# Optimization experiments

Hardware: AMD Instinct MI355X
Metric: run time of the kernel (lower is better)

## Reference

```python
import jax, jax.numpy as jnp
import numpy as np

B, D, L, NH = 8, 1024, 1024, 8
DK = D // NH  # = Dv = 128
NEG = -1e30


def setup_inputs() -> dict:
    key = jax.random.key(0)
    kx, km, kq, kk, kv, ko = jax.random.split(key, 6)
    x = jax.random.normal(kx, (B, D, L), dtype=jnp.float32)
    # binary mask over sequence positions (float, as in the torch code)
    mask = (jax.random.uniform(km, (B, L)) > 0.1).astype(jnp.float32)
    # xavier-ish scale for per-head projections, kaiming-ish for Wo
    s_qkv = np.sqrt(2.0 / (D + DK)).astype(np.float32)
    Wq = jax.random.normal(kq, (NH, D, DK), dtype=jnp.float32) * s_qkv
    Wk = jax.random.normal(kk, (NH, D, DK), dtype=jnp.float32) * s_qkv
    Wv = jax.random.normal(kv, (NH, D, DK), dtype=jnp.float32) * s_qkv
    Wo = jax.random.normal(ko, (D, DK * NH), dtype=jnp.float32) * np.sqrt(2.0 / D).astype(np.float32)
    return {"x": x, "mask": mask, "Wq": Wq, "Wk": Wk, "Wv": Wv, "Wo": Wo}


def reference(x, mask, Wq, Wk, Wv, Wo):
    # x: [B, D, L] -> [B, L, D]
    xt = jnp.swapaxes(x, 1, 2)
    scale = 1.0 / np.sqrt(DK).astype(np.float32)
    # batched per-head projections (equivalent to the per-head loop)
    q = jnp.einsum("bld,hdk->bhlk", xt, Wq)  # [B,H,L,Dk]
    k = jnp.einsum("bld,hdk->bhlk", xt, Wk)
    v = jnp.einsum("bld,hdk->bhlk", xt, Wv)
    # scores[b,h,q_pos,k_pos]
    scores = jnp.einsum("bhqd,bhkd->bhqk", q, k) * scale
    # mask.unsqueeze(2) in torch -> additive mask along the QUERY axis
    scores = scores + (1.0 - mask)[:, None, :, None] * NEG
    # faithful quirk: softmax over dim=1 of [B,Lq,Lk] == query axis (axis=2 here)
    attn = jax.nn.softmax(scores, axis=2)
    heads = jnp.einsum("bhqk,bhkd->bhqd", attn, v)  # [B,H,L,Dv]
    head = jnp.swapaxes(heads, 1, 2).reshape(B, L, NH * DK)  # concat heads
    out = head @ Wo  # [B, L, D]
    return jnp.swapaxes(out, 1, 2)  # [B, D, L]
```

## Files before the change

kernel.cpp:

```cpp
#include <hip/hip_runtime.h>

typedef short bf16x8 __attribute__((ext_vector_type(8)));
typedef float f32x4 __attribute__((ext_vector_type(4)));

#define MASK_NEG (-1e30f)

__device__ __forceinline__ unsigned short f2bf(float f) {
  union { float f; unsigned u; } v; v.f = f;
  unsigned r = v.u + 0x7fffu + ((v.u >> 16) & 1u);
  return (unsigned short)(r >> 16);
}

__device__ __forceinline__ float bf2f(unsigned short u) {
  union { unsigned u; float f; } v; v.u = ((unsigned)u) << 16;
  return v.f;
}

__device__ __forceinline__ void gl_lds16(const void* g, void* l) {
  __builtin_amdgcn_global_load_lds(
      (__attribute__((address_space(1))) void*)(void*)g,
      (__attribute__((address_space(3))) void*)l, 16, 0, 0);
}

__device__ __forceinline__ void transpose_tile(
    const float* __restrict__ s, unsigned short* __restrict__ d,
    int R, int C, int x0, int y0, int t, float tile[64][65]) {
  {
    const int r = t >> 4, c4 = (t & 15) * 4;
    for (int it = 0; it < 4; ++it) {
      const int rr = r + it * 16;
      const float4 v = *(const float4*)(s + (size_t)(y0 + rr) * C + x0 + c4);
      tile[rr][c4 + 0] = v.x; tile[rr][c4 + 1] = v.y;
      tile[rr][c4 + 2] = v.z; tile[rr][c4 + 3] = v.w;
    }
  }
  __syncthreads();
  {
    const int cc = t >> 4, r4 = (t & 15) * 4;
    for (int it = 0; it < 4; ++it) {
      const int c = cc + it * 16;
      ushort4 o;
      o.x = f2bf(tile[r4 + 0][c]); o.y = f2bf(tile[r4 + 1][c]);
      o.z = f2bf(tile[r4 + 2][c]); o.w = f2bf(tile[r4 + 3][c]);
      *(ushort4*)(d + (size_t)(x0 + c) * R + y0 + r4) = o;
    }
  }
}

__global__ __launch_bounds__(256) void transpose_x_wo(
    const float* __restrict__ x, const float* __restrict__ Wo,
    unsigned short* __restrict__ xt, unsigned short* __restrict__ Wot) {
  __shared__ float tile[64][65];
  const int z = blockIdx.z;
  const float* s = (z < 8) ? (x + (size_t)z * 1048576) : Wo;
  unsigned short* d = (z < 8) ? (xt + (size_t)z * 1048576) : Wot;
  transpose_tile(s, d, 1024, 1024, blockIdx.x * 64, blockIdx.y * 64,
                 threadIdx.x, tile);
}

__global__ __launch_bounds__(256) void transpose_w24(
    const float* __restrict__ Wq, const float* __restrict__ Wk,
    const float* __restrict__ Wv, unsigned short* __restrict__ WqkvT) {
  __shared__ float tile[64][65];
  const int z = blockIdx.z;
  const int sel = z >> 3, h = z & 7;
  const float* base = (sel == 0) ? Wq : (sel == 1) ? Wk : Wv;
  const float* s = base + (size_t)h * 131072;
  unsigned short* d = WqkvT + (size_t)z * 131072;
  transpose_tile(s, d, 1024, 128, blockIdx.x * 64, blockIdx.y * 64,
                 threadIdx.x, tile);
}

template<bool F32OUT>
__global__ __launch_bounds__(256) void gemm_tn(
    const unsigned short* __restrict__ A, const unsigned short* __restrict__ B,
    void* __restrict__ Cv,
    int K, int ldA, int ldB, int ldC, float scale,
    long sAl, long sAb, long sAh,
    long sBl, long sBb, long sBh,
    long sCl, long sCb, long sCh,
    int zbase, int zdiv)
{
  __shared__ unsigned short As[128 * 64];
  __shared__ unsigned short Bs[128 * 64];
  int bx, by, bz;
  {
    const int nx = gridDim.x, ny = gridDim.y;
    const int nwg = nx * ny * gridDim.z;
    int flat = blockIdx.x + nx * (blockIdx.y + ny * blockIdx.z);
    if ((nwg & 7) == 0) flat = (flat & 7) * (nwg >> 3) + (flat >> 3);
    bx = flat % nx; flat /= nx;
    by = flat % ny; bz = flat / ny;
  }
  const int z = bz;
  const int g = zbase + z;
  const int gb = g / zdiv, gh = g % zdiv;
  const unsigned short* Ab = A + (size_t)z * sAl + (size_t)gb * sAb + (size_t)gh * sAh;
  const unsigned short* Bb = B + (size_t)z * sBl + (size_t)gb * sBb + (size_t)gh * sBh;
  const int m0 = by * 128, n0 = bx * 128;
  const int t = threadIdx.x;
  const int lane = t & 63;
  const int wave = t >> 6;
  const int wm = wave >> 1, wn = wave & 1;

  const int sr2 = t >> 3;
  const int ss8 = t & 7;
  const int sq8 = ss8 ^ (sr2 & 7);

  const unsigned short* ap0 = Ab + (size_t)(m0 +  0 + sr2) * ldA + sq8 * 8;
  const unsigned short* ap1 = Ab + (size_t)(m0 + 32 + sr2) * ldA + sq8 * 8;
  const unsigned short* ap2 = Ab + (size_t)(m0 + 64 + sr2) * ldA + sq8 * 8;
  const unsigned short* ap3 = Ab + (size_t)(m0 + 96 + sr2) * ldA + sq8 * 8;
  const unsigned short* bp0 = Bb + (size_t)(n0 +  0 + sr2) * ldB + sq8 * 8;
  const unsigned short* bp1 = Bb + (size_t)(n0 + 32 + sr2) * ldB + sq8 * 8;
  const unsigned short* bp2 = Bb + (size_t)(n0 + 64 + sr2) * ldB + sq8 * 8;
  const unsigned short* bp3 = Bb + (size_t)(n0 + 96 + sr2) * ldB + sq8 * 8;

  char* asd0 = (char*)As +     0 + t * 16;
  char* asd1 = (char*)As +  4096 + t * 16;
  char* asd2 = (char*)As +  8192 + t * 16;
  char* asd3 = (char*)As + 12288 + t * 16;
  char* bsd0 = (char*)Bs +     0 + t * 16;
  char* bsd1 = (char*)Bs +  4096 + t * 16;
  char* bsd2 = (char*)Bs +  8192 + t * 16;
  char* bsd3 = (char*)Bs + 12288 + t * 16;

  const int tq = lane & 15, qd = lane >> 4;

  f32x4 acc[4][4];
  #pragma unroll
  for (int i = 0; i < 4; ++i)
    #pragma unroll
    for (int j = 0; j < 4; ++j)
      acc[i][j] = f32x4{0.f, 0.f, 0.f, 0.f};

  const int kIters = K >> 6;
  for (int kt = 0; kt < kIters; ++kt) {
    __syncthreads();
    gl_lds16(ap0, asd0); gl_lds16(ap1, asd1);
    gl_lds16(ap2, asd2); gl_lds16(ap3, asd3);
    gl_lds16(bp0, bsd0); gl_lds16(bp1, bsd1);
    gl_lds16(bp2, bsd2); gl_lds16(bp3, bsd3);
    ap0 += 64; ap1 += 64; ap2 += 64; ap3 += 64;
    bp0 += 64; bp1 += 64; bp2 += 64; bp3 += 64;
    __builtin_amdgcn_s_waitcnt(0x0f70);
    __syncthreads();

    #pragma unroll
    for (int kk = 0; kk < 2; ++kk) {
      bf16x8 af[4], bfr[4];
      #pragma unroll
      for (int i = 0; i < 4; ++i) {
        const int R = wm * 64 + i * 16 + tq;
        const int slot = (kk * 4 + qd) ^ (R & 7);
        af[i] = *(const bf16x8*)(As + R * 64 + slot * 8);
      }
      #pragma unroll
      for (int j = 0; j < 4; ++j) {
        const int R = wn * 64 + j * 16 + tq;
        const int slot = (kk * 4 + qd) ^ (R & 7);
        bfr[j] = *(const bf16x8*)(Bs + R * 64 + slot * 8);
      }
      #pragma unroll
      for (int i = 0; i < 4; ++i)
        #pragma unroll
        for (int j = 0; j < 4; ++j)
          acc[i][j] = __builtin_amdgcn_mfma_f32_16x16x32_bf16(af[i], bfr[j], acc[i][j], 0, 0, 0);
    }
  }

  const size_t cOff = (size_t)z * sCl + (size_t)gb * sCb + (size_t)gh * sCh;
  #pragma unroll
  for (int i = 0; i < 4; ++i) {
    const int row = m0 + wm * 64 + i * 16 + qd * 4;
    #pragma unroll
    for (int j = 0; j < 4; ++j) {
      const int col = n0 + wn * 64 + j * 16 + tq;
      if constexpr (F32OUT) {
        float* C = (float*)Cv + cOff;
        #pragma unroll
        for (int rr = 0; rr < 4; ++rr)
          C[(size_t)(row + rr) * ldC + col] = acc[i][j][rr] * scale;
      } else {
        unsigned short* C = (unsigned short*)Cv + cOff;
        #pragma unroll
        for (int rr = 0; rr < 4; ++rr)
          C[(size_t)(row + rr) * ldC + col] = f2bf(acc[i][j][rr] * scale);
      }
    }
  }
}

__global__ __launch_bounds__(256) void gemm_scores_colsum(
    const unsigned short* __restrict__ QKV, float* __restrict__ colsum,
    const float* __restrict__ mask)
{
  __shared__ unsigned short sbuf[32768];
  unsigned short* As = sbuf;
  unsigned short* Bs = sbuf + 16384;
  int flat = blockIdx.x + 8 * (blockIdx.y + 8 * blockIdx.z);
  flat = (flat & 7) * 512 + (flat >> 3);
  const int bx = flat & 7, by = (flat >> 3) & 7, g = flat >> 6;
  const int b = g >> 3, h = g & 7;
  const unsigned short* Ab = QKV + (size_t)b * 3145728 + (size_t)h * 131072;
  const unsigned short* Bb = Ab + 1048576;
  const int m0 = by * 128, n0 = bx * 128;
  const int t = threadIdx.x;
  const int lane = t & 63;
  const int wave = t >> 6;
  const int wm = wave >> 1, wn = wave & 1;
  const int tq = lane & 15, qd = lane >> 4;

  const unsigned short* Aq = Ab + (size_t)m0 * 128;
  const unsigned short* Bk = Bb + (size_t)n0 * 128;
  #pragma unroll
  for (int it = 0; it < 8; ++it) {
    const int c = it * 256 + t;
    const int row = c >> 4;
    const int src = (c ^ (c >> 4)) & 15;
    gl_lds16(Aq + (size_t)row * 128 + src * 8, (char*)As + c * 16);
    gl_lds16(Bk + (size_t)row * 128 + src * 8, (char*)Bs + c * 16);
  }
  __builtin_amdgcn_s_waitcnt(0x0f70);
  __syncthreads();

  f32x4 acc[4][4];
  #pragma unroll
  for (int i = 0; i < 4; ++i)
    #pragma unroll
    for (int j = 0; j < 4; ++j)
      acc[i][j] = f32x4{0.f, 0.f, 0.f, 0.f};

  #pragma unroll
  for (int kk = 0; kk < 4; ++kk) {
    bf16x8 af[4], bfr[4];
    #pragma unroll
    for (int i = 0; i < 4; ++i) {
      const int R = wm * 64 + i * 16 + tq;
      const int slot = (kk * 4 + qd) ^ (R & 15);
      af[i] = *(const bf16x8*)(As + R * 128 + slot * 8);
    }
    #pragma unroll
    for (int j = 0; j < 4; ++j) {
      const int R = wn * 64 + j * 16 + tq;
      const int slot = (kk * 4 + qd) ^ (R & 15);
      bfr[j] = *(const bf16x8*)(Bs + R * 128 + slot * 8);
    }
    #pragma unroll
    for (int i = 0; i < 4; ++i)
      #pragma unroll
      for (int j = 0; j < 4; ++j)
        acc[i][j] = __builtin_amdgcn_mfma_f32_16x16x32_bf16(af[i], bfr[j], acc[i][j], 0, 0, 0);
  }

  float* cs = colsum + (size_t)g * 1024;
  const float scl = 0.08838834764831845f;
  const float* mrow = mask + (size_t)b * 1024;

  float cp[4] = {0.f, 0.f, 0.f, 0.f};
  #pragma unroll
  for (int i = 0; i < 4; ++i) {
    const int r0 = wm * 64 + i * 16 + qd * 4;
    const float4 m4 = *(const float4*)(mrow + m0 + r0);
    const float aq[4] = {(1.f - m4.x) * MASK_NEG - 20.f, (1.f - m4.y) * MASK_NEG - 20.f,
                         (1.f - m4.z) * MASK_NEG - 20.f, (1.f - m4.w) * MASK_NEG - 20.f};
    #pragma unroll
    for (int rr = 0; rr < 4; ++rr) {
      #pragma unroll
      for (int j = 0; j < 4; ++j) {
        const float e = __expf(acc[i][j][rr] * scl + aq[rr]);
        cp[j] += e;
      }
    }
  }
  #pragma unroll
  for (int j = 0; j < 4; ++j) {
    float v = cp[j];
    v += __shfl_xor(v, 16, 64);
    v += __shfl_xor(v, 32, 64);
    if (qd == 0)
      atomicAdd(&cs[n0 + wn * 64 + j * 16 + tq], v);
  }
}

__global__ __launch_bounds__(256) void tvscale(
    const unsigned short* __restrict__ QKV, unsigned short* __restrict__ Vp,
    const float* __restrict__ colsum)
{
  __shared__ unsigned short tile[64][72];
  const int g = blockIdx.z;
  const int b = g >> 3, h = g & 7;
  const unsigned short* S = QKV + (size_t)b * 3145728 + (size_t)(16 + h) * 131072;
  unsigned short* D = Vp + (size_t)g * 131072;
  const float* cs = colsum + (size_t)g * 1024;
  const int l0 = blockIdx.x * 64;
  const int d0 = blockIdx.y * 64;
  const int t = threadIdx.x;
  {
    const int r = t >> 4, c4 = (t & 15) * 4;
    for (int it = 0; it < 4; ++it) {
      const int rr = r + it * 16;
      const ushort4 v = *(const ushort4*)(S + (size_t)(l0 + rr) * 128 + d0 + c4);
      *(ushort4*)&tile[rr][c4] = v;
    }
  }
  __syncthreads();
  {
    const int cc = t >> 4, r4 = (t & 15) * 4;
    const float4 c4v = *(const float4*)(cs + l0 + r4);
    for (int it = 0; it < 4; ++it) {
      const int c = cc + it * 16;
      ushort4 o;
      o.x = f2bf(bf2f(tile[r4 + 0][c]) / c4v.x);
      o.y = f2bf(bf2f(tile[r4 + 1][c]) / c4v.y);
      o.z = f2bf(bf2f(tile[r4 + 2][c]) / c4v.z);
      o.w = f2bf(bf2f(tile[r4 + 3][c]) / c4v.w);
      *(ushort4*)(D + (size_t)(d0 + c) * 1024 + l0 + r4) = o;
    }
  }
}

__global__ __launch_bounds__(256, 2) void attn_pv_fused(
    const unsigned short* __restrict__ QKV, const unsigned short* __restrict__ Vp,
    unsigned short* __restrict__ Hp, const float* __restrict__ mask)
{
  __shared__ unsigned short lds[32768];
  unsigned short* Qs = lds;
  unsigned short* Ps = lds;
  unsigned short* Ks = lds + 16384;
  unsigned short* Vs = lds + 24576;

  const int bid = blockIdx.x;
  const int w = ((bid & 7) << 6) | (bid >> 3);
  const int g = w >> 3, qx = w & 7;
  const int b = g >> 3, h = g & 7;
  const unsigned short* Qg = QKV + (size_t)b * 3145728 + (size_t)h * 131072
                                 + (size_t)qx * 16384;
  const unsigned short* Kg = QKV + (size_t)b * 3145728 + (size_t)(8 + h) * 131072;
  const unsigned short* Vg = Vp + (size_t)g * 131072;

  const int t = threadIdx.x;
  const int lane = t & 63, wave = t >> 6;
  const int wm = wave >> 1, wn = wave & 1;
  const int tq = lane & 15, qd = lane >> 4;

  #pragma unroll
  for (int it = 0; it < 8; ++it) {
    const int c = it * 256 + t;
    const int row = c >> 4;
    const int src = (c ^ (c >> 4)) & 15;
    gl_lds16(Qg + (size_t)row * 128 + src * 8, (char*)Qs + c * 16);
  }
  __builtin_amdgcn_s_waitcnt(0x0f70);
  __syncthreads();

  bf16x8 qf[4][4];
  #pragma unroll
  for (int i = 0; i < 4; ++i) {
    const int R = wm * 64 + i * 16 + tq;
    #pragma unroll
    for (int kk = 0; kk < 4; ++kk)
      qf[i][kk] = *(const bf16x8*)(Qs + R * 128 + (((kk * 4 + qd) ^ (R & 15)) * 8));
  }
  __syncthreads();

  f32x4 acc_h[4][4];
  #pragma unroll
  for (int i = 0; i < 4; ++i)
    #pragma unroll
    for (int j = 0; j < 4; ++j)
      acc_h[i][j] = f32x4{0.f, 0.f, 0.f, 0.f};

  const float scl = 0.08838834764831845f;
  float aq[4][4];
  {
    const float* mrow = mask + (size_t)b * 1024 + qx * 128;
    #pragma unroll
    for (int i = 0; i < 4; ++i) {
      const float4 m4 = *(const float4*)(mrow + wm * 64 + i * 16 + qd * 4);
      aq[i][0] = (1.f - m4.x) * MASK_NEG - 20.f;
      aq[i][1] = (1.f - m4.y) * MASK_NEG - 20.f;
      aq[i][2] = (1.f - m4.z) * MASK_NEG - 20.f;
      aq[i][3] = (1.f - m4.w) * MASK_NEG - 20.f;
    }
  }

  for (int kt = 0; kt < 16; ++kt) {
    __syncthreads();
    #pragma unroll
    for (int it = 0; it < 4; ++it) {
      const int c = it * 256 + t;
      const int row = c >> 4;
      const int src = (c ^ (c >> 4)) & 15;
      gl_lds16(Kg + (size_t)(kt * 64 + row) * 128 + src * 8, (char*)Ks + c * 16);
    }
    #pragma unroll
    for (int it = 0; it < 4; ++it) {
      const int c = it * 256 + t;
      const int row = c >> 3;
      const int src = (c ^ (c >> 3)) & 7;
      gl_lds16(Vg + (size_t)row * 1024 + kt * 64 + src * 8, (char*)Vs + c * 16);
    }
    __builtin_amdgcn_s_waitcnt(0x0f70);
    __syncthreads();

    f32x4 acc_s[4][2];
    #pragma unroll
    for (int i = 0; i < 4; ++i)
      #pragma unroll
      for (int j = 0; j < 2; ++j)
        acc_s[i][j] = f32x4{0.f, 0.f, 0.f, 0.f};
    #pragma unroll
    for (int kk = 0; kk < 4; ++kk) {
      bf16x8 kf[2];
      #pragma unroll
      for (int j = 0; j < 2; ++j) {
        const int R = wn * 32 + j * 16 + tq;
        kf[j] = *(const bf16x8*)(Ks + R * 128 + (((kk * 4 + qd) ^ (R & 15)) * 8));
      }
      #pragma unroll
      for (int i = 0; i < 4; ++i)
        #pragma unroll
        for (int j = 0; j < 2; ++j)
          acc_s[i][j] = __builtin_amdgcn_mfma_f32_16x16x32_bf16(qf[i][kk], kf[j], acc_s[i][j], 0, 0, 0);
    }

    #pragma unroll
    for (int i = 0; i < 4; ++i) {
      const int q0 = wm * 64 + i * 16 + qd * 4;
      #pragma unroll
      for (int rr = 0; rr < 4; ++rr) {
        const int q = q0 + rr;
        #pragma unroll
        for (int j = 0; j < 2; ++j) {
          const int kl = wn * 32 + j * 16 + tq;
          const float e = __expf(acc_s[i][j][rr] * scl + aq[i][rr]);
          Ps[q * 64 + ((((kl >> 3) ^ (q & 7)) * 8) | (kl & 7))] = f2bf(e);
        }
      }
    }
    __syncthreads();

    #pragma unroll
    for (int k2 = 0; k2 < 2; ++k2) {
      bf16x8 pf[4], vf[4];
      #pragma unroll
      for (int i = 0; i < 4; ++i) {
        const int R = wm * 64 + i * 16 + tq;
        pf[i] = *(const bf16x8*)(Ps + R * 64 + (((k2 * 4 + qd) ^ (R & 7)) * 8));
      }
      #pragma unroll
      for (int j = 0; j < 4; ++j) {
        const int R = wn * 64 + j * 16 + tq;
        vf[j] = *(const bf16x8*)(Vs + R * 64 + (((k2 * 4 + qd) ^ (R & 7)) * 8));
      }
      #pragma unroll
      for (int i = 0; i < 4; ++i)
        #pragma unroll
        for (int j = 0; j < 4; ++j)
          acc_h[i][j] = __builtin_amdgcn_mfma_f32_16x16x32_bf16(pf[i], vf[j], acc_h[i][j], 0, 0, 0);
    }
  }

  unsigned short* Hb = Hp + (size_t)b * 1048576 + (size_t)qx * 131072 + h * 128;
  #pragma unroll
  for (int i = 0; i < 4; ++i) {
    const int q0 = wm * 64 + i * 16 + qd * 4;
    #pragma unroll
    for (int j = 0; j < 4; ++j) {
      const int dv = wn * 64 + j * 16 + tq;
      #pragma unroll
      for (int rr = 0; rr < 4; ++rr)
        Hb[(size_t)(q0 + rr) * 1024 + dv] = f2bf(acc_h[i][j][rr]);
    }
  }
}

extern "C" void kernel_launch(void* const* d_in, const int* in_sizes, int n_in,
                              void* d_out, int out_size, void* d_ws, size_t ws_size,
                              hipStream_t stream) {
  const float* x    = (const float*)d_in[0];
  const float* mask = (const float*)d_in[1];
  const float* Wq   = (const float*)d_in[2];
  const float* Wk   = (const float*)d_in[3];
  const float* Wv   = (const float*)d_in[4];
  const float* Wo   = (const float*)d_in[5];
  float* out = (float*)d_out;

  char* p = (char*)d_ws;
  unsigned short* xt    = (unsigned short*)p; p += 16777216;
  unsigned short* WqkvT = (unsigned short*)p; p += 6291456;
  unsigned short* Wot   = (unsigned short*)p; p += 2097152;
  unsigned short* QKV   = (unsigned short*)p; p += 50331648;
  unsigned short* Vp    = (unsigned short*)p; p += 16777216;
  unsigned short* Hp    = (unsigned short*)p; p += 16777216;
  float* colsum = (float*)p; p += 262144;

  hipMemsetAsync(colsum, 0, 262144, stream);

  transpose_x_wo<<<dim3(16, 16, 9), 256, 0, stream>>>(x, Wo, xt, Wot);
  transpose_w24<<<dim3(2, 16, 24), 256, 0, stream>>>(Wq, Wk, Wv, WqkvT);

  gemm_tn<false><<<dim3(1, 8, 192), 256, 0, stream>>>(
      xt, WqkvT, (void*)QKV, 1024, 1024, 1024, 128, 1.f,
      0L, 1048576L, 0L,  0L, 0L, 131072L,  0L, 3145728L, 131072L, 0, 24);

  gemm_scores_colsum<<<dim3(8, 8, 64), 256, 0, stream>>>(QKV, colsum, mask);

  tvscale<<<dim3(16, 2, 64), 256, 0, stream>>>(QKV, Vp, colsum);

  attn_pv_fused<<<dim3(512, 1, 1), 256, 0, stream>>>(QKV, Vp, Hp, mask);

  gemm_tn<true><<<dim3(8, 8, 8), 256, 0, stream>>>(
      Wot, Hp, (void*)out, 1024, 1024, 1024, 1024, 1.f,
      0L, 0L, 0L,  0L, 1048576L, 0L,  0L, 1048576L, 0L, 0, 1);
}
```

Measured before the change: 276.2 us.

## Fuse V transpose into QKV GEMM and fold colsum scaling into attention

The QKV projection GEMM now writes V directly in transposed layout, so the separate tvscale kernel goes away. The per-key column-sum normalization moves into the attention kernel, which multiplies each exp by the reciprocal colsum. The scores/colsum kernel is restructured to loop over K tiles per query block with double-buffered loads, and the attention kernel double-buffers its K/V loads to overlap them with compute. The costs are more LDS per block, uncoalesced ushort4 transposed stores in the GEMM epilogue, and more atomics per block in the colsum pass.

```diff
diff --git a/kernel.cpp b/kernel.cpp
--- a/kernel.cpp
+++ b/kernel.cpp
@@ -9,11 +9,6 @@
   union { float f; unsigned u; } v; v.f = f;
   unsigned r = v.u + 0x7fffu + ((v.u >> 16) & 1u);
   return (unsigned short)(r >> 16);
-}
-
-__device__ __forceinline__ float bf2f(unsigned short u) {
-  union { unsigned u; float f; } v; v.u = ((unsigned)u) << 16;
-  return v.f;
 }
 
 __device__ __forceinline__ void gl_lds16(const void* g, void* l) {
@@ -79,7 +74,7 @@
     long sAl, long sAb, long sAh,
     long sBl, long sBb, long sBh,
     long sCl, long sCb, long sCh,
-    int zbase, int zdiv)
+    int zbase, int zdiv, unsigned short* __restrict__ Vt)
 {
   __shared__ unsigned short As[128 * 64];
   __shared__ unsigned short Bs[128 * 64];
@@ -169,6 +164,25 @@
     }
   }
 
+  if (!F32OUT && Vt != nullptr && gh >= 16) {
+    unsigned short* Vb = Vt + (size_t)(gb * 8 + (gh - 16)) * 131072;
+    #pragma unroll
+    for (int i = 0; i < 4; ++i) {
+      const int row = m0 + wm * 64 + i * 16 + qd * 4;
+      #pragma unroll
+      for (int j = 0; j < 4; ++j) {
+        const int col = n0 + wn * 64 + j * 16 + tq;
+        ushort4 o;
+        o.x = f2bf(acc[i][j][0] * scale);
+        o.y = f2bf(acc[i][j][1] * scale);
+        o.z = f2bf(acc[i][j][2] * scale);
+        o.w = f2bf(acc[i][j][3] * scale);
+        *(ushort4*)(Vb + (size_t)col * 1024 + row) = o;
+      }
+    }
+    return;
+  }
+
   const size_t cOff = (size_t)z * sCl + (size_t)gb * sCb + (size_t)gh * sCh;
   #pragma unroll
   for (int i = 0; i < 4; ++i) {
@@ -191,144 +205,133 @@
   }
 }
 
-__global__ __launch_bounds__(256) void gemm_scores_colsum(
+__global__ __launch_bounds__(256, 2) void scores_colsum(
     const unsigned short* __restrict__ QKV, float* __restrict__ colsum,
     const float* __restrict__ mask)
 {
-  __shared__ unsigned short sbuf[32768];
-  unsigned short* As = sbuf;
-  unsigned short* Bs = sbuf + 16384;
-  int flat = blockIdx.x + 8 * (blockIdx.y + 8 * blockIdx.z);
-  flat = (flat & 7) * 512 + (flat >> 3);
-  const int bx = flat & 7, by = (flat >> 3) & 7, g = flat >> 6;
+  __shared__ unsigned short lds[24576];
+  unsigned short* Qs = lds;
+
+  const int bid = blockIdx.x;
+  const int w = ((bid & 7) << 6) | (bid >> 3);
+  const int g = w >> 3, qx = w & 7;
   const int b = g >> 3, h = g & 7;
-  const unsigned short* Ab = QKV + (size_t)b * 3145728 + (size_t)h * 131072;
-  const unsigned short* Bb = Ab + 1048576;
-  const int m0 = by * 128, n0 = bx * 128;
+  const unsigned short* Qg = QKV + (size_t)b * 3145728 + (size_t)h * 131072
+                                 + (size_t)qx * 16384;
+  const unsigned short* Kg = QKV + (size_t)b * 3145728 + (size_t)(8 + h) * 131072;
+
   const int t = threadIdx.x;
-  const int lane = t & 63;
-  const int wave = t >> 6;
+  const int lane = t & 63, wave = t >> 6;
   const int wm = wave >> 1, wn = wave & 1;
   const int tq = lane & 15, qd = lane >> 4;
 
-  const unsigned short* Aq = Ab + (size_t)m0 * 128;
-  const unsigned short* Bk = Bb + (size_t)n0 * 128;
   #pragma unroll
   for (int it = 0; it < 8; ++it) {
     const int c = it * 256 + t;
     const int row = c >> 4;
     const int src = (c ^ (c >> 4)) & 15;
-    gl_lds16(Aq + (size_t)row * 128 + src * 8, (char*)As + c * 16);
-    gl_lds16(Bk + (size_t)row * 128 + src * 8, (char*)Bs + c * 16);
+    gl_lds16(Qg + (size_t)row * 128 + src * 8, (char*)Qs + c * 16);
+  }
+  #pragma unroll
+  for (int it = 0; it < 4; ++it) {
+    const int c = it * 256 + t;
+    const int row = c >> 4;
+    const int src = (c ^ (c >> 4)) & 15;
+    gl_lds16(Kg + (size_t)row * 128 + src * 8, (char*)(lds + 16384) + c * 16);
   }
   __builtin_amdgcn_s_waitcnt(0x0f70);
   __syncthreads();
 
-  f32x4 acc[4][4];
-  #pragma unroll
-  for (int i = 0; i < 4; ++i)
-    #pragma unroll
-    for (int j = 0; j < 4; ++j)
-      acc[i][j] = f32x4{0.f, 0.f, 0.f, 0.f};
-
-  #pragma unroll
-  for (int kk = 0; kk < 4; ++kk) {
-    bf16x8 af[4], bfr[4];
+  bf16x8 qf[4][4];
+  #pragma unroll
+  for (int i = 0; i < 4; ++i) {
+    const int R = wm * 64 + i * 16 + tq;
+    #pragma unroll
+    for (int kk = 0; kk < 4; ++kk)
+      qf[i][kk] = *(const bf16x8*)(Qs + R * 128 + (((kk * 4 + qd) ^ (R & 15)) * 8));
+  }
+  __syncthreads();
+
+  const float scl = 0.08838834764831845f;
+  float aq[4][4];
+  {
+    const float* mrow = mask + (size_t)b * 1024 + qx * 128;
     #pragma unroll
     for (int i = 0; i < 4; ++i) {
-      const int R = wm * 64 + i * 16 + tq;
-      const int slot = (kk * 4 + qd) ^ (R & 15);
-      af[i] = *(const bf16x8*)(As + R * 128 + slot * 8);
-    }
-    #pragma unroll
-    for (int j = 0; j < 4; ++j) {
-      const int R = wn * 64 + j * 16 + tq;
-      const int slot = (kk * 4 + qd) ^ (R & 15);
-      bfr[j] = *(const bf16x8*)(Bs + R * 128 + slot * 8);
-    }
+      const float4 m4 = *(const float4*)(mrow + wm * 64 + i * 16 + qd * 4);
+      aq[i][0] = (1.f - m4.x) * MASK_NEG - 20.f;
+      aq[i][1] = (1.f - m4.y) * MASK_NEG - 20.f;
+      aq[i][2] = (1.f - m4.z) * MASK_NEG - 20.f;
+      aq[i][3] = (1.f - m4.w) * MASK_NEG - 20.f;
+    }
+  }
+  float* cs = colsum + (size_t)g * 1024;
+
+  for (int kt = 0; kt < 16; ++kt) {
+    __syncthreads();
+    if (kt < 15) {
+      unsigned short* Kn = ((kt + 1) & 1) ? lds : (lds + 16384);
+      const unsigned short* Kgn = Kg + (size_t)(kt + 1) * 64 * 128;
+      #pragma unroll
+      for (int it = 0; it < 4; ++it) {
+        const int c = it * 256 + t;
+        const int row = c >> 4;
+        const int src = (c ^ (c >> 4)) & 15;
+        gl_lds16(Kgn + (size_t)row * 128 + src * 8, (char*)Kn + c * 16);
+      }
+      __builtin_amdgcn_s_waitcnt(0x0f74);
+    } else {
+      __builtin_amdgcn_s_waitcnt(0x0f70);
+    }
+    __syncthreads();
+
+    const unsigned short* Kc = (kt & 1) ? lds : (lds + 16384);
+    f32x4 acc_s[4][2];
     #pragma unroll
     for (int i = 0; i < 4; ++i)
       #pragma unroll
-      for (int j = 0; j < 4; ++j)
-        acc[i][j] = __builtin_amdgcn_mfma_f32_16x16x32_bf16(af[i], bfr[j], acc[i][j], 0, 0, 0);
-  }
-
-  float* cs = colsum + (size_t)g * 1024;
-  const float scl = 0.08838834764831845f;
-  const float* mrow = mask + (size_t)b * 1024;
-
-  float cp[4] = {0.f, 0.f, 0.f, 0.f};
-  #pragma unroll
-  for (int i = 0; i < 4; ++i) {
-    const int r0 = wm * 64 + i * 16 + qd * 4;
-    const float4 m4 = *(const float4*)(mrow + m0 + r0);
-    const float aq[4] = {(1.f - m4.x) * MASK_NEG - 20.f, (1.f - m4.y) * MASK_NEG - 20.f,
-                         (1.f - m4.z) * MASK_NEG - 20.f, (1.f - m4.w) * MASK_NEG - 20.f};
-    #pragma unroll
-    for (int rr = 0; rr < 4; ++rr) {
-      #pragma unroll
-      for (int j = 0; j < 4; ++j) {
-        const float e = __expf(acc[i][j][rr] * scl + aq[rr]);
-        cp[j] += e;
-      }
-    }
-  }
-  #pragma unroll
-  for (int j = 0; j < 4; ++j) {
-    float v = cp[j];
-    v += __shfl_xor(v, 16, 64);
-    v += __shfl_xor(v, 32, 64);
-    if (qd == 0)
-      atomicAdd(&cs[n0 + wn * 64 + j * 16 + tq], v);
-  }
-}
-
-__global__ __launch_bounds__(256) void tvscale(
-    const unsigned short* __restrict__ QKV, unsigned short* __restrict__ Vp,
+      for (int j = 0; j < 2; ++j)
+        acc_s[i][j] = f32x4{0.f, 0.f, 0.f, 0.f};
+    #pragma unroll
+    for (int kk = 0; kk < 4; ++kk) {
+      bf16x8 kf[2];
+      #pragma unroll
+      for (int j = 0; j < 2; ++j) {
+        const int R = wn * 32 + j * 16 + tq;
+        kf[j] = *(const bf16x8*)(Kc + R * 128 + (((kk * 4 + qd) ^ (R & 15)) * 8));
+      }
+      #pragma unroll
+      for (int i = 0; i < 4; ++i)
+        #pragma unroll
+        for (int j = 0; j < 2; ++j)
+          acc_s[i][j] = __builtin_amdgcn_mfma_f32_16x16x32_bf16(qf[i][kk], kf[j], acc_s[i][j], 0, 0, 0);
+    }
+
+    float cp0 = 0.f, cp1 = 0.f;
+    #pragma unroll
+    for (int i = 0; i < 4; ++i)
+      #pragma unroll
+      for (int rr = 0; rr < 4; ++rr) {
+        cp0 += __expf(acc_s[i][0][rr] * scl + aq[i][rr]);
+        cp1 += __expf(acc_s[i][1][rr] * scl + aq[i][rr]);
+      }
+    cp0 += __shfl_xor(cp0, 16, 64); cp0 += __shfl_xor(cp0, 32, 64);
+    cp1 += __shfl_xor(cp1, 16, 64); cp1 += __shfl_xor(cp1, 32, 64);
+    if (qd == 0) {
+      atomicAdd(&cs[kt * 64 + wn * 32 + tq], cp0);
+      atomicAdd(&cs[kt * 64 + wn * 32 + 16 + tq], cp1);
+    }
+  }
+}
+
+__global__ __launch_bounds__(256, 2) void attn_pv_fused(
+    const unsigned short* __restrict__ QKV, const unsigned short* __restrict__ Vp,
+    unsigned short* __restrict__ Hp, const float* __restrict__ mask,
     const float* __restrict__ colsum)
 {
-  __shared__ unsigned short tile[64][72];
-  const int g = blockIdx.z;
-  const int b = g >> 3, h = g & 7;
-  const unsigned short* S = QKV + (size_t)b * 3145728 + (size_t)(16 + h) * 131072;
-  unsigned short* D = Vp + (size_t)g * 131072;
-  const float* cs = colsum + (size_t)g * 1024;
-  const int l0 = blockIdx.x * 64;
-  const int d0 = blockIdx.y * 64;
-  const int t = threadIdx.x;
-  {
-    const int r = t >> 4, c4 = (t & 15) * 4;
-    for (int it = 0; it < 4; ++it) {
-      const int rr = r + it * 16;
-      const ushort4 v = *(const ushort4*)(S + (size_t)(l0 + rr) * 128 + d0 + c4);
-      *(ushort4*)&tile[rr][c4] = v;
-    }
-  }
-  __syncthreads();
-  {
-    const int cc = t >> 4, r4 = (t & 15) * 4;
-    const float4 c4v = *(const float4*)(cs + l0 + r4);
-    for (int it = 0; it < 4; ++it) {
-      const int c = cc + it * 16;
-      ushort4 o;
-      o.x = f2bf(bf2f(tile[r4 + 0][c]) / c4v.x);
-      o.y = f2bf(bf2f(tile[r4 + 1][c]) / c4v.y);
-      o.z = f2bf(bf2f(tile[r4 + 2][c]) / c4v.z);
-      o.w = f2bf(bf2f(tile[r4 + 3][c]) / c4v.w);
-      *(ushort4*)(D + (size_t)(d0 + c) * 1024 + l0 + r4) = o;
-    }
-  }
-}
-
-__global__ __launch_bounds__(256, 2) void attn_pv_fused(
-    const unsigned short* __restrict__ QKV, const unsigned short* __restrict__ Vp,
-    unsigned short* __restrict__ Hp, const float* __restrict__ mask)
-{
-  __shared__ unsigned short lds[32768];
+  __shared__ unsigned short lds[40960];
+  unsigned short* Ps = lds;
   unsigned short* Qs = lds;
-  unsigned short* Ps = lds;
-  unsigned short* Ks = lds + 16384;
-  unsigned short* Vs = lds + 24576;
 
   const int bid = blockIdx.x;
   const int w = ((bid & 7) << 6) | (bid >> 3);
@@ -351,6 +354,20 @@
     const int src = (c ^ (c >> 4)) & 15;
     gl_lds16(Qg + (size_t)row * 128 + src * 8, (char*)Qs + c * 16);
   }
+  #pragma unroll
+  for (int it = 0; it < 4; ++it) {
+    const int c = it * 256 + t;
+    const int row = c >> 4;
+    const int src = (c ^ (c >> 4)) & 15;
+    gl_lds16(Kg + (size_t)row * 128 + src * 8, (char*)(lds + 16384) + c * 16);
+  }
+  #pragma unroll
+  for (int it = 0; it < 4; ++it) {
+    const int c = it * 256 + t;
+    const int row = c >> 3;
+    const int src = (c ^ (c >> 3)) & 7;
+    gl_lds16(Vg + (size_t)row * 1024 + src * 8, (char*)(lds + 24576) + c * 16);
+  }
   __builtin_amdgcn_s_waitcnt(0x0f70);
   __syncthreads();
 
@@ -384,25 +401,36 @@
       aq[i][3] = (1.f - m4.w) * MASK_NEG - 20.f;
     }
   }
+  const float* cs = colsum + (size_t)g * 1024;
 
   for (int kt = 0; kt < 16; ++kt) {
     __syncthreads();
-    #pragma unroll
-    for (int it = 0; it < 4; ++it) {
-      const int c = it * 256 + t;
-      const int row = c >> 4;
-      const int src = (c ^ (c >> 4)) & 15;
-      gl_lds16(Kg + (size_t)(kt * 64 + row) * 128 + src * 8, (char*)Ks + c * 16);
-    }
-    #pragma unroll
-    for (int it = 0; it < 4; ++it) {
-      const int c = it * 256 + t;
-      const int row = c >> 3;
-      const int src = (c ^ (c >> 3)) & 7;
-      gl_lds16(Vg + (size_t)row * 1024 + kt * 64 + src * 8, (char*)Vs + c * 16);
-    }
-    __builtin_amdgcn_s_waitcnt(0x0f70);
-    __syncthreads();
+    if (kt < 15) {
+      unsigned short* Kn = ((kt + 1) & 1) ? (lds + 8192) : (lds + 16384);
+      unsigned short* Vn = ((kt + 1) & 1) ? (lds + 32768) : (lds + 24576);
+      const unsigned short* Kgn = Kg + (size_t)(kt + 1) * 64 * 128;
+      #pragma unroll
+      for (int it = 0; it < 4; ++it) {
+        const int c = it * 256 + t;
+        const int row = c >> 4;
+        const int src = (c ^ (c >> 4)) & 15;
+        gl_lds16(Kgn + (size_t)row * 128 + src * 8, (char*)Kn + c * 16);
+      }
+      #pragma unroll
+      for (int it = 0; it < 4; ++it) {
+        const int c = it * 256 + t;
+        const int row = c >> 3;
+        const int src = (c ^ (c >> 3)) & 7;
+        gl_lds16(Vg + (size_t)row * 1024 + (kt + 1) * 64 + src * 8, (char*)Vn + c * 16);
+      }
+      __builtin_amdgcn_s_waitcnt(0x0f78);
+    } else {
+      __builtin_amdgcn_s_waitcnt(0x0f70);
+    }
+    __syncthreads();
+
+    const unsigned short* Kc = (kt & 1) ? (lds + 8192) : (lds + 16384);
+    const unsigned short* Vc = (kt & 1) ? (lds + 32768) : (lds + 24576);
 
     f32x4 acc_s[4][2];
     #pragma unroll
@@ -416,7 +444,7 @@
       #pragma unroll
       for (int j = 0; j < 2; ++j) {
         const int R = wn * 32 + j * 16 + tq;
-        kf[j] = *(const bf16x8*)(Ks + R * 128 + (((kk * 4 + qd) ^ (R & 15)) * 8));
+        kf[j] = *(const bf16x8*)(Kc + R * 128 + (((kk * 4 + qd) ^ (R & 15)) * 8));
       }
       #pragma unroll
       for (int i = 0; i < 4; ++i)
@@ -425,6 +453,8 @@
           acc_s[i][j] = __builtin_amdgcn_mfma_f32_16x16x32_bf16(qf[i][kk], kf[j], acc_s[i][j], 0, 0, 0);
     }
 
+    const float rcs0 = 1.0f / cs[kt * 64 + wn * 32 + tq];
+    const float rcs1 = 1.0f / cs[kt * 64 + wn * 32 + 16 + tq];
     #pragma unroll
     for (int i = 0; i < 4; ++i) {
       const int q0 = wm * 64 + i * 16 + qd * 4;
@@ -434,7 +464,7 @@
         #pragma unroll
         for (int j = 0; j < 2; ++j) {
           const int kl = wn * 32 + j * 16 + tq;
-          const float e = __expf(acc_s[i][j][rr] * scl + aq[i][rr]);
+          const float e = __expf(acc_s[i][j][rr] * scl + aq[i][rr]) * (j ? rcs1 : rcs0);
           Ps[q * 64 + ((((kl >> 3) ^ (q & 7)) * 8) | (kl & 7))] = f2bf(e);
         }
       }
@@ -452,7 +482,7 @@
       #pragma unroll
       for (int j = 0; j < 4; ++j) {
         const int R = wn * 64 + j * 16 + tq;
-        vf[j] = *(const bf16x8*)(Vs + R * 64 + (((k2 * 4 + qd) ^ (R & 7)) * 8));
+        vf[j] = *(const bf16x8*)(Vc + R * 64 + (((k2 * 4 + qd) ^ (R & 7)) * 8));
       }
       #pragma unroll
       for (int i = 0; i < 4; ++i)
@@ -503,15 +533,13 @@
 
   gemm_tn<false><<<dim3(1, 8, 192), 256, 0, stream>>>(
       xt, WqkvT, (void*)QKV, 1024, 1024, 1024, 128, 1.f,
-      0L, 1048576L, 0L,  0L, 0L, 131072L,  0L, 3145728L, 131072L, 0, 24);
-
-  gemm_scores_colsum<<<dim3(8, 8, 64), 256, 0, stream>>>(QKV, colsum, mask);
-
-  tvscale<<<dim3(16, 2, 64), 256, 0, stream>>>(QKV, Vp, colsum);
-
-  attn_pv_fused<<<dim3(512, 1, 1), 256, 0, stream>>>(QKV, Vp, Hp, mask);
+      0L, 1048576L, 0L,  0L, 0L, 131072L,  0L, 3145728L, 131072L, 0, 24, Vp);
+
+  scores_colsum<<<dim3(512, 1, 1), 256, 0, stream>>>(QKV, colsum, mask);
+
+  attn_pv_fused<<<dim3(512, 1, 1), 256, 0, stream>>>(QKV, Vp, Hp, mask, colsum);
 
   gemm_tn<true><<<dim3(8, 8, 8), 256, 0, stream>>>(
       Wot, Hp, (void*)out, 1024, 1024, 1024, 1024, 1.f,
-      0L, 0L, 0L,  0L, 1048576L, 0L,  0L, 1048576L, 0L, 0, 1);
-}
+      0L, 0L, 0L,  0L, 1048576L, 0L,  0L, 1048576L, 0L, 0, 1, nullptr);
+}
```

Result: slower. 285.2 us (+3.3%).
